# Kernel optimization log

Measured on AMD Instinct MI355X. Metric: run time of the kernel, lower is better.

The kernel has to match this reference:

```python
import jax, jax.numpy as jnp
import numpy as np

HIDDEN_DIM = 256
ATTN_DIM = 256


def setup_inputs() -> dict:
    key = jax.random.key(0)
    k1, k2, k3, k4, k5, k6 = jax.random.split(key, 6)
    B, S, C, H, W = 16, 32, HIDDEN_DIM, 16, 16
    hidden_state = jax.random.normal(k1, (B, C, H, W), dtype=jnp.float32)
    encoder_outputs = jax.random.normal(k2, (B, S, C, H, W), dtype=jnp.float32)
    # 1x1 conv weights stored as [out_ch, in_ch] (kernel spatial dims are 1)
    W1 = jax.random.normal(k3, (ATTN_DIM, 2 * C), dtype=jnp.float32) * (1.0 / np.sqrt(2 * C))
    b1 = jax.random.normal(k4, (ATTN_DIM,), dtype=jnp.float32) * 0.01
    W2 = jax.random.normal(k5, (1, ATTN_DIM), dtype=jnp.float32) * (1.0 / np.sqrt(ATTN_DIM))
    b2 = jax.random.normal(k6, (1,), dtype=jnp.float32) * 0.01
    return {"hidden_state": hidden_state, "encoder_outputs": encoder_outputs,
            "W1": W1, "b1": b1, "W2": W2, "b2": b2}


def reference(hidden_state, encoder_outputs, W1, b1, W2, b2):
    # hidden_state: [B, C, H, W]; encoder_outputs: [B, S, C, H, W]
    C = hidden_state.shape[1]
    # conv1(cat(h_expanded, e)) decomposed: W1 = [W1h | W1e] over channel dim.
    W1h, W1e = W1[:, :C], W1[:, C:]
    # [B, A, H, W] broadcast over S + [B, S, A, H, W]
    eh = jnp.einsum('ac,bchw->bahw', W1h, hidden_state)
    ee = jnp.einsum('ac,bschw->bsahw', W1e, encoder_outputs)
    t = jnp.tanh(eh[:, None] + ee + b1[None, None, :, None, None])
    # conv2 -> [B, S, H, W], then spatial mean -> [B, S]
    energy = jnp.einsum('a,bsahw->bshw', W2[0], t) + b2[0]
    energy = energy.reshape(energy.shape[0], energy.shape[1], -1).mean(axis=2)
    attn_weights = jax.nn.softmax(energy, axis=1)  # [B, S]
    context = jnp.einsum('bs,bschw->bchw', attn_weights, encoder_outputs)
    return context
```

## Files before the change

kernel.cpp:

```cpp
#include <hip/hip_runtime.h>

#define P 256
#define CDIM 256
#define SDIM 32

typedef __attribute__((ext_vector_type(8))) short short8;
typedef __attribute__((ext_vector_type(4))) float f32x4;
typedef __attribute__((ext_vector_type(4))) unsigned int uint4v;

__device__ inline unsigned int pack2bf(float lo, float hi) {
    unsigned int ul = __builtin_bit_cast(unsigned int, lo);
    unsigned int uh = __builtin_bit_cast(unsigned int, hi);
    ul += 0x7fffu + ((ul >> 16) & 1u);
    uh += 0x7fffu + ((uh >> 16) & 1u);
    return (ul >> 16) | (uh & 0xffff0000u);
}

__global__ __launch_bounds__(256) void prep_kernel(const float* __restrict__ hid,
                                                   const float* __restrict__ W1,
                                                   const float* __restrict__ b1,
                                                   float* __restrict__ ehb1,
                                                   uint4v* __restrict__ packA) {
    const int blk = blockIdx.x;
    const int tid = threadIdx.x;
    if (blk >= 1024) {
        const int t  = (blk - 1024) * 256 + tid;
        const int a  = ((t >> 9) << 4) | (t & 15);
        const int kc = (t >> 4) & 31;
        const float* src = W1 + (size_t)a * 512 + 256 + kc * 8;
        const float4 f0 = *(const float4*)src;
        const float4 f1 = *(const float4*)(src + 4);
        uint4v u;
        u.x = pack2bf(f0.x, f0.y);
        u.y = pack2bf(f0.z, f0.w);
        u.z = pack2bf(f1.x, f1.y);
        u.w = pack2bf(f1.z, f1.w);
        packA[t] = u;
        return;
    }
    const int b  = blk >> 6;
    const int a0 = (blk & 63) << 2;
    const int p  = tid;
    float acc[4];
#pragma unroll
    for (int i = 0; i < 4; ++i) acc[i] = 0.f;
    const float* hb = hid + (size_t)b * CDIM * P;
    for (int c = 0; c < CDIM; c += 8) {
        float hv[8];
#pragma unroll
        for (int j = 0; j < 8; ++j) hv[j] = hb[(c + j) * P + p];
#pragma unroll
        for (int i = 0; i < 4; ++i) {
            const float* wr = W1 + (size_t)(a0 + i) * 512 + c;
#pragma unroll
            for (int j = 0; j < 8; ++j) acc[i] = fmaf(wr[j], hv[j], acc[i]);
        }
    }
#pragma unroll
    for (int i = 0; i < 4; ++i)
        ehb1[((size_t)b * CDIM + a0 + i) * P + p] = acc[i] + b1[a0 + i];
}

__global__ __launch_bounds__(256, 2) void energy_mfma(const float* __restrict__ enc,
                                                      const unsigned char* __restrict__ packA,
                                                      const float* __restrict__ W2,
                                                      const float* __restrict__ ehb1,
                                                      float* __restrict__ partial) {
    __shared__ __align__(16) unsigned char bufF[3][64 * 256];
    __shared__ __align__(16) unsigned char ldsB[64 * 128];
    __shared__ float red[4];
    const int bid = blockIdx.x;
    const int bs  = bid >> 2;
    const int pq  = bid & 3;
    const int b   = bs >> 5;
    const int tid = threadIdx.x;
    const int l   = tid & 63;
    const int w   = tid >> 6;
    const int g   = l >> 4;
    const int i16 = l & 15;
    const int a_base = w * 64;
    const int p_r = tid & 63;
    const int ch  = tid >> 6;
    const float* eb   = enc  + (size_t)bs * (CDIM * P) + pq * 64;
    const float* ehbB = ehb1 + (size_t)b  * (CDIM * P) + pq * 64;

#define DMA_TILE(KT, BUF)                                                          \
    {                                                                              \
        const float* gsrc = eb + (size_t)((KT) * 64 + w * 16) * P;                 \
        unsigned char* ldst = (BUF) + (w * 16) * 256;                              \
        _Pragma("unroll")                                                          \
        for (int i_ = 0; i_ < 4; ++i_) {                                           \
            __builtin_amdgcn_global_load_lds(                                      \
                (const unsigned int*)(gsrc + (size_t)(i_ * 4 + (l >> 4)) * P +     \
                                      (l & 15) * 4),                               \
                (unsigned int*)(ldst + i_ * 1024), 16, 0, 0);                      \
        }                                                                          \
    }

#define TRANSPOSE(BUF)                                                             \
    {                                                                              \
        float cv[16];                                                              \
        _Pragma("unroll")                                                          \
        for (int j_ = 0; j_ < 16; ++j_)                                            \
            cv[j_] = *(const float*)((BUF) + (ch * 16 + j_) * 256 + p_r * 4);      \
        unsigned char* dst = ldsB + p_r * 128;                                     \
        _Pragma("unroll")                                                          \
        for (int h_ = 0; h_ < 2; ++h_) {                                           \
            uint4v u;                                                              \
            u.x = pack2bf(cv[h_*8+0], cv[h_*8+1]);                                 \
            u.y = pack2bf(cv[h_*8+2], cv[h_*8+3]);                                 \
            u.z = pack2bf(cv[h_*8+4], cv[h_*8+5]);                                 \
            u.w = pack2bf(cv[h_*8+6], cv[h_*8+7]);                                 \
            *(uint4v*)(dst + ((ch * 32 + h_ * 16) ^ ((p_r & 7) << 4))) = u;        \
        }                                                                          \
    }

    f32x4 acc[4][4];
    float w2v[4][4];
#pragma unroll
    for (int m = 0; m < 4; ++m) {
#pragma unroll
        for (int r = 0; r < 4; ++r) {
            const int a = a_base + m * 16 + g * 4 + r;
            w2v[m][r] = W2[a];
            const float* ehr = ehbB + (size_t)a * P + i16;
#pragma unroll
            for (int n = 0; n < 4; ++n)
                acc[m][n][r] = ehr[n * 16];
        }
    }
    __builtin_amdgcn_sched_barrier(0);
    DMA_TILE(0, bufF[0]);
    DMA_TILE(1, bufF[1]);
    __builtin_amdgcn_sched_barrier(0);
    short8 af[2][2][4];
#pragma unroll
    for (int kh = 0; kh < 2; ++kh)
#pragma unroll
        for (int m = 0; m < 4; ++m) {
            const int chunk = ((a_base >> 4) + m) * 32 + 0 * 8 + kh * 4;
            af[0][kh][m] = __builtin_bit_cast(short8,
                *(const uint4v*)(packA + (size_t)chunk * 256 + l * 16));
        }
    __builtin_amdgcn_sched_barrier(0);
    asm volatile("s_waitcnt vmcnt(12)" ::: "memory");
    __builtin_amdgcn_sched_barrier(0);
    __builtin_amdgcn_s_barrier();
    TRANSPOSE(bufF[0]);
    asm volatile("s_waitcnt lgkmcnt(0)" ::: "memory");
    __builtin_amdgcn_sched_barrier(0);
    __builtin_amdgcn_s_barrier();

#pragma unroll
    for (int kt = 0; kt < 4; ++kt) {
        if (kt < 2) DMA_TILE(kt + 2, bufF[(kt + 2) % 3]);
        __builtin_amdgcn_sched_barrier(0);
        if (kt < 3) {
#pragma unroll
            for (int kh = 0; kh < 2; ++kh)
#pragma unroll
                for (int m = 0; m < 4; ++m) {
                    const int chunk = ((a_base >> 4) + m) * 32 + (kt + 1) * 8 + kh * 4;
                    af[(kt + 1) & 1][kh][m] = __builtin_bit_cast(short8,
                        *(const uint4v*)(packA + (size_t)chunk * 256 + l * 16));
                }
        }
        __builtin_amdgcn_sched_barrier(0);
#pragma unroll
        for (int kh = 0; kh < 2; ++kh) {
            short8 bf[4];
#pragma unroll
            for (int n = 0; n < 4; ++n) {
                const int row = n * 16 + i16;
                bf[n] = __builtin_bit_cast(short8,
                    *(const uint4v*)(ldsB + row * 128 +
                                     (((kh * 4 + g) * 16) ^ ((row & 7) << 4))));
            }
#pragma unroll
            for (int m = 0; m < 4; ++m)
#pragma unroll
                for (int n = 0; n < 4; ++n)
                    acc[m][n] = __builtin_amdgcn_mfma_f32_16x16x32_bf16(af[kt & 1][kh][m], bf[n], acc[m][n], 0, 0, 0);
        }
        if (kt == 0 || kt == 1) {
            asm volatile("s_waitcnt vmcnt(12)" ::: "memory");
        } else if (kt == 2) {
            asm volatile("s_waitcnt vmcnt(8)" ::: "memory");
        }
        if (kt < 3) {
            __builtin_amdgcn_sched_barrier(0);
            __builtin_amdgcn_s_barrier();
            TRANSPOSE(bufF[(kt + 1) % 3]);
            asm volatile("s_waitcnt lgkmcnt(0)" ::: "memory");
            __builtin_amdgcn_sched_barrier(0);
            __builtin_amdgcn_s_barrier();
        }
    }
#undef DMA_TILE
#undef TRANSPOSE

    float epm[4];
#pragma unroll
    for (int m = 0; m < 4; ++m) {
        float e = 0.f;
#pragma unroll
        for (int r = 0; r < 4; ++r) {
            const float wv = w2v[m][r];
#pragma unroll
            for (int n = 0; n < 4; ++n) {
                const float x  = acc[m][n][r];
                const float ex = __expf(2.f * x);
                const float t  = 1.f - 2.f / (ex + 1.f);
                e = fmaf(wv, t, e);
            }
        }
        epm[m] = e;
    }
    float ep = (epm[0] + epm[1]) + (epm[2] + epm[3]);
#pragma unroll
    for (int off = 32; off > 0; off >>= 1) ep += __shfl_down(ep, off, 64);
    if (l == 0) red[w] = ep;
    __syncthreads();
    if (tid == 0)
        partial[(size_t)bs * 4 + pq] = red[0] + red[1] + red[2] + red[3];
}

__global__ __launch_bounds__(256) void context_kernel(const float4* __restrict__ enc4,
                                                      const float* __restrict__ partial,
                                                      const float* __restrict__ b2,
                                                      float4* __restrict__ out4) {
    const int bi = blockIdx.x;
    const int b  = bi >> 6;
    const int i4 = ((bi & 63) << 8) + threadIdx.x;

    float e[SDIM];
    const float* pb = partial + (size_t)b * SDIM * 4;
    const float bias = b2[0];
#pragma unroll
    for (int s = 0; s < SDIM; ++s)
        e[s] = (pb[s*4] + pb[s*4+1] + pb[s*4+2] + pb[s*4+3]) * (1.f / 256.f) + bias;
    float m = e[0];
#pragma unroll
    for (int s = 1; s < SDIM; ++s) m = fmaxf(m, e[s]);
    float sum = 0.f;
#pragma unroll
    for (int s = 0; s < SDIM; ++s) { e[s] = __expf(e[s] - m); sum += e[s]; }
    const float inv = 1.f / sum;

    float4 acc = {0.f, 0.f, 0.f, 0.f};
    const float4* eb = enc4 + (size_t)b * SDIM * 16384 + i4;
#pragma unroll 4
    for (int s = 0; s < SDIM; ++s) {
        const float wv = e[s] * inv;
        const float4 v = eb[(size_t)s * 16384];
        acc.x = fmaf(wv, v.x, acc.x);
        acc.y = fmaf(wv, v.y, acc.y);
        acc.z = fmaf(wv, v.z, acc.z);
        acc.w = fmaf(wv, v.w, acc.w);
    }
    out4[(size_t)b * 16384 + i4] = acc;
}

extern "C" void kernel_launch(void* const* d_in, const int* in_sizes, int n_in,
                              void* d_out, int out_size, void* d_ws, size_t ws_size,
                              hipStream_t stream) {
    const float* hid = (const float*)d_in[0];
    const float* enc = (const float*)d_in[1];
    const float* W1  = (const float*)d_in[2];
    const float* b1  = (const float*)d_in[3];
    const float* W2  = (const float*)d_in[4];
    const float* b2  = (const float*)d_in[5];
    float* out = (float*)d_out;

    float* ehb1    = out;
    float* partial = (float*)d_ws;
    unsigned char* packA = (unsigned char*)(partial + 2048);

    prep_kernel<<<1056, 256, 0, stream>>>(hid, W1, b1, ehb1, (uint4v*)packA);
    energy_mfma<<<2048, 256, 0, stream>>>(enc, packA, W2, ehb1, partial);
    context_kernel<<<1024, 256, 0, stream>>>((const float4*)enc, partial, b2, (float4*)out);
}
```

Before: 92.16 us.

## Drop triple-buffered LDS pipeline for single buffer and higher occupancy

Replaces the three-slot LDS staging buffer and its hand-scheduled prefetch, with manual waitcnt and sched_barrier, by a single tile buffer. Each k-step now transposes, syncs, issues the next tile's DMA, and runs the MFMAs. The A fragments are loaded per k-half instead of double-buffered, and W2 is read in the epilogue. Launch bounds rise from 2 to 4 blocks per CU, cutting LDS and register use to fit more resident blocks. The cost is less latency hiding within a block and extra full barriers per iteration.

```diff
diff --git a/kernel.cpp b/kernel.cpp
--- a/kernel.cpp
+++ b/kernel.cpp
@@ -61,12 +61,12 @@
         ehb1[((size_t)b * CDIM + a0 + i) * P + p] = acc[i] + b1[a0 + i];
 }
 
-__global__ __launch_bounds__(256, 2) void energy_mfma(const float* __restrict__ enc,
+__global__ __launch_bounds__(256, 4) void energy_mfma(const float* __restrict__ enc,
                                                       const unsigned char* __restrict__ packA,
                                                       const float* __restrict__ W2,
                                                       const float* __restrict__ ehb1,
                                                       float* __restrict__ partial) {
-    __shared__ __align__(16) unsigned char bufF[3][64 * 256];
+    __shared__ __align__(16) unsigned char bufF[64 * 256];
     __shared__ __align__(16) unsigned char ldsB[64 * 128];
     __shared__ float red[4];
     const int bid = blockIdx.x;
@@ -84,10 +84,10 @@
     const float* eb   = enc  + (size_t)bs * (CDIM * P) + pq * 64;
     const float* ehbB = ehb1 + (size_t)b  * (CDIM * P) + pq * 64;
 
-#define DMA_TILE(KT, BUF)                                                          \
+#define DMA_TILE(KT)                                                               \
     {                                                                              \
         const float* gsrc = eb + (size_t)((KT) * 64 + w * 16) * P;                 \
-        unsigned char* ldst = (BUF) + (w * 16) * 256;                              \
+        unsigned char* ldst = bufF + (w * 16) * 256;                               \
         _Pragma("unroll")                                                          \
         for (int i_ = 0; i_ < 4; ++i_) {                                           \
             __builtin_amdgcn_global_load_lds(                                      \
@@ -97,12 +97,12 @@
         }                                                                          \
     }
 
-#define TRANSPOSE(BUF)                                                             \
+#define TRANSPOSE()                                                                \
     {                                                                              \
         float cv[16];                                                              \
         _Pragma("unroll")                                                          \
         for (int j_ = 0; j_ < 16; ++j_)                                            \
-            cv[j_] = *(const float*)((BUF) + (ch * 16 + j_) * 256 + p_r * 4);      \
+            cv[j_] = *(const float*)(bufF + (ch * 16 + j_) * 256 + p_r * 4);       \
         unsigned char* dst = ldsB + p_r * 128;                                     \
         _Pragma("unroll")                                                          \
         for (int h_ = 0; h_ < 2; ++h_) {                                           \
@@ -115,60 +115,35 @@
         }                                                                          \
     }
 
+    DMA_TILE(0);
     f32x4 acc[4][4];
-    float w2v[4][4];
 #pragma unroll
     for (int m = 0; m < 4; ++m) {
 #pragma unroll
         for (int r = 0; r < 4; ++r) {
             const int a = a_base + m * 16 + g * 4 + r;
-            w2v[m][r] = W2[a];
             const float* ehr = ehbB + (size_t)a * P + i16;
 #pragma unroll
             for (int n = 0; n < 4; ++n)
                 acc[m][n][r] = ehr[n * 16];
         }
     }
-    __builtin_amdgcn_sched_barrier(0);
-    DMA_TILE(0, bufF[0]);
-    DMA_TILE(1, bufF[1]);
-    __builtin_amdgcn_sched_barrier(0);
-    short8 af[2][2][4];
-#pragma unroll
-    for (int kh = 0; kh < 2; ++kh)
-#pragma unroll
-        for (int m = 0; m < 4; ++m) {
-            const int chunk = ((a_base >> 4) + m) * 32 + 0 * 8 + kh * 4;
-            af[0][kh][m] = __builtin_bit_cast(short8,
-                *(const uint4v*)(packA + (size_t)chunk * 256 + l * 16));
-        }
-    __builtin_amdgcn_sched_barrier(0);
-    asm volatile("s_waitcnt vmcnt(12)" ::: "memory");
-    __builtin_amdgcn_sched_barrier(0);
-    __builtin_amdgcn_s_barrier();
-    TRANSPOSE(bufF[0]);
-    asm volatile("s_waitcnt lgkmcnt(0)" ::: "memory");
-    __builtin_amdgcn_sched_barrier(0);
-    __builtin_amdgcn_s_barrier();
+    __syncthreads();
 
 #pragma unroll
     for (int kt = 0; kt < 4; ++kt) {
-        if (kt < 2) DMA_TILE(kt + 2, bufF[(kt + 2) % 3]);
-        __builtin_amdgcn_sched_barrier(0);
-        if (kt < 3) {
-#pragma unroll
-            for (int kh = 0; kh < 2; ++kh)
-#pragma unroll
-                for (int m = 0; m < 4; ++m) {
-                    const int chunk = ((a_base >> 4) + m) * 32 + (kt + 1) * 8 + kh * 4;
-                    af[(kt + 1) & 1][kh][m] = __builtin_bit_cast(short8,
-                        *(const uint4v*)(packA + (size_t)chunk * 256 + l * 16));
-                }
-        }
-        __builtin_amdgcn_sched_barrier(0);
+        TRANSPOSE();
+        __syncthreads();
+        if (kt < 3) DMA_TILE(kt + 1);
 #pragma unroll
         for (int kh = 0; kh < 2; ++kh) {
-            short8 bf[4];
+            short8 af[4], bf[4];
+#pragma unroll
+            for (int m = 0; m < 4; ++m) {
+                const int chunk = ((a_base >> 4) + m) * 32 + kt * 8 + kh * 4;
+                af[m] = __builtin_bit_cast(short8,
+                    *(const uint4v*)(packA + (size_t)chunk * 256 + l * 16));
+            }
 #pragma unroll
             for (int n = 0; n < 4; ++n) {
                 const int row = n * 16 + i16;
@@ -180,21 +155,9 @@
             for (int m = 0; m < 4; ++m)
 #pragma unroll
                 for (int n = 0; n < 4; ++n)
-                    acc[m][n] = __builtin_amdgcn_mfma_f32_16x16x32_bf16(af[kt & 1][kh][m], bf[n], acc[m][n], 0, 0, 0);
-        }
-        if (kt == 0 || kt == 1) {
-            asm volatile("s_waitcnt vmcnt(12)" ::: "memory");
-        } else if (kt == 2) {
-            asm volatile("s_waitcnt vmcnt(8)" ::: "memory");
-        }
-        if (kt < 3) {
-            __builtin_amdgcn_sched_barrier(0);
-            __builtin_amdgcn_s_barrier();
-            TRANSPOSE(bufF[(kt + 1) % 3]);
-            asm volatile("s_waitcnt lgkmcnt(0)" ::: "memory");
-            __builtin_amdgcn_sched_barrier(0);
-            __builtin_amdgcn_s_barrier();
-        }
+                    acc[m][n] = __builtin_amdgcn_mfma_f32_16x16x32_bf16(af[m], bf[n], acc[m][n], 0, 0, 0);
+        }
+        __syncthreads();
     }
 #undef DMA_TILE
 #undef TRANSPOSE
@@ -205,7 +168,7 @@
         float e = 0.f;
 #pragma unroll
         for (int r = 0; r < 4; ++r) {
-            const float wv = w2v[m][r];
+            const float wv = W2[a_base + m * 16 + g * 4 + r];
 #pragma unroll
             for (int n = 0; n < 4; ++n) {
                 const float x  = acc[m][n][r];
```

New measurement: 91.65 us. No clear change (-0.6%).
